# Kernel tuning notes

Measured on AMD Instinct MI355X. Metric: run time of the kernel, lower is better.

Reference implementation:

```python
import jax, jax.numpy as jnp
import numpy as np

B, S, H, V = 32, 128, 1024, 32000


def setup_inputs() -> dict:
    key = jax.random.key(0)
    ks = jax.random.split(key, 20)
    sc = 1.0 / np.sqrt(H)
    inp = {
        "inputs": jax.random.randint(ks[0], (B, S), 0, V),
        "annotations": jax.random.normal(ks[1], (B, S, H), dtype=jnp.float32),
        "hidden_init": jax.random.normal(ks[2], (B, H), dtype=jnp.float32),
        "E": jax.random.normal(ks[3], (V, H), dtype=jnp.float32) * sc,
        "Wxr": jax.random.normal(ks[4], (H, H), dtype=jnp.float32) * sc,
        "bxr": jnp.zeros((H,), jnp.float32),
        "Wxz": jax.random.normal(ks[5], (H, H), dtype=jnp.float32) * sc,
        "bxz": jnp.zeros((H,), jnp.float32),
        "Wxg": jax.random.normal(ks[6], (H, H), dtype=jnp.float32) * sc,
        "bxg": jnp.zeros((H,), jnp.float32),
        "Whr": jax.random.normal(ks[7], (H, H), dtype=jnp.float32) * sc,
        "bhr": jnp.zeros((H,), jnp.float32),
        "Whz": jax.random.normal(ks[8], (H, H), dtype=jnp.float32) * sc,
        "bhz": jnp.zeros((H,), jnp.float32),
        "Whg": jax.random.normal(ks[9], (H, H), dtype=jnp.float32) * sc,
        "bhg": jnp.zeros((H,), jnp.float32),
        "Wout": jax.random.normal(ks[10], (H, V), dtype=jnp.float32) * sc,
        "bout": jnp.zeros((V,), jnp.float32),
    }
    return inp


def reference(inputs, annotations, hidden_init, E, Wxr, bxr, Wxz, bxz, Wxg, bxg,
              Whr, bhr, Whz, bhz, Whg, bhg, Wout, bout):
    # annotations is unused (matches original non-attentional decoder).
    emb = E[inputs]  # [B, S, H]
    # Precompute all input-to-hidden projections as batched GEMMs (time-parallel).
    xr = jnp.einsum('bsh,hk->bsk', emb, Wxr) + bxr  # [B,S,H]
    xz = jnp.einsum('bsh,hk->bsk', emb, Wxz) + bxz
    xg = jnp.einsum('bsh,hk->bsk', emb, Wxg) + bxg
    # Scan over time for the sequential recurrence.
    xs = (jnp.swapaxes(xr, 0, 1), jnp.swapaxes(xz, 0, 1), jnp.swapaxes(xg, 0, 1))  # [S,B,H]

    def step(h, x):
        x_r, x_z, x_g = x
        r = jax.nn.sigmoid(x_r + h @ Whr + bhr)
        z = jax.nn.sigmoid(x_z + h @ Whz + bhz)
        g = jnp.tanh(x_g + r * (h @ Whg + bhg))
        h_new = (1.0 - z) * g + z * h
        return h_new, h_new

    _, hiddens = jax.lax.scan(step, hidden_init, xs)  # [S,B,H]
    hiddens = jnp.swapaxes(hiddens, 0, 1)  # [B,S,H]
    output = jnp.einsum('bsh,hv->bsv', hiddens, Wout) + bout  # [B,S,V]
    return output
```

## Files before the change

kernel.cpp:

```cpp
#include <hip/hip_runtime.h>
#include <hip/hip_bf16.h>

#define B_ 32
#define S_ 128
#define H_ 1024
#define V_ 32000

using short8 = __attribute__((ext_vector_type(8))) short;
using f32x4  = __attribute__((ext_vector_type(4))) float;
typedef unsigned short u16;

__device__ inline u16 f2bf(float f) {
  unsigned u = __float_as_uint(f);
  unsigned r = u + 0x7FFFu + ((u >> 16) & 1u);
  return (u16)(r >> 16);
}
__device__ inline float bf2f(u16 h) { return __uint_as_float(((unsigned)h) << 16); }

__device__ inline void gload_lds16(const void* g, void* l) {
  __builtin_amdgcn_global_load_lds((const __attribute__((address_space(1))) unsigned int*)g,
                                   (__attribute__((address_space(3))) unsigned int*)l, 16, 0, 0);
}
__device__ inline void gload_lds16_sc(const void* g, void* l) {
  __builtin_amdgcn_global_load_lds((const __attribute__((address_space(1))) unsigned int*)g,
                                   (__attribute__((address_space(3))) unsigned int*)l, 16, 0, 17);
}


__global__ void k_gather_embed(const int* __restrict__ idx, const float* __restrict__ E,
                               u16* __restrict__ embf) {
  int g = blockIdx.x * blockDim.x + threadIdx.x;
  int kt = g >> 14, rem = g & 16383, mt = rem >> 6, l = rem & 63;
  int row = mt * 16 + (l & 15);
  int k = kt * 32 + ((l >> 4) << 3);
  const float4* src = reinterpret_cast<const float4*>(E + (size_t)idx[row] * H_ + k);
  float4 a = src[0], b = src[1];
  u16 o[8] = {f2bf(a.x), f2bf(a.y), f2bf(a.z), f2bf(a.w),
              f2bf(b.x), f2bf(b.y), f2bf(b.z), f2bf(b.w)};
  *reinterpret_cast<uint4*>(embf + (size_t)g * 8) = *reinterpret_cast<const uint4*>(o);
}

__global__ void k_cvt_wx(const float* __restrict__ Wxr, const float* __restrict__ Wxz,
                         const float* __restrict__ Wxg, u16* __restrict__ wxf) {
  int g = blockIdx.x * blockDim.x + threadIdx.x;
  int kt = g / 12288, rem = g % 12288, nf = rem >> 6, l = rem & 63;
  int col = nf * 16 + (l & 15);
  int gate = col >> 10, j = col & 1023;
  int k0 = kt * 32 + ((l >> 4) << 3);
  const float* W = gate == 0 ? Wxr : (gate == 1 ? Wxz : Wxg);
  u16 o[8];
#pragma unroll
  for (int e = 0; e < 8; ++e) o[e] = f2bf(W[(size_t)(k0 + e) * H_ + j]);
  *reinterpret_cast<uint4*>(wxf + (size_t)g * 8) = *reinterpret_cast<const uint4*>(o);
}

__global__ void k_cvt_wout(const float* __restrict__ W, u16* __restrict__ wof) {
  int g = blockIdx.x * blockDim.x + threadIdx.x;
  int kt = g / 128000, rem = g - kt * 128000, nf = rem >> 6, l = rem & 63;
  int col = nf * 16 + (l & 15);
  int k0 = kt * 32 + ((l >> 4) << 3);
  u16 o[8];
#pragma unroll
  for (int e = 0; e < 8; ++e) o[e] = f2bf(W[(size_t)(k0 + e) * V_ + col]);
  *reinterpret_cast<uint4*>(wof + (size_t)g * 8) = *reinterpret_cast<const uint4*>(o);
}

__global__ void k_prep_wh(const float* __restrict__ Whr, const float* __restrict__ Whz,
                          const float* __restrict__ Whg, u16* __restrict__ whh,
                          u16* __restrict__ whl) {
  int g = blockIdx.x * blockDim.x + threadIdx.x;
  int jtile = g / 6144, rem = g % 6144;
  int gate = rem >> 11, kt = (rem >> 6) & 31, l = rem & 63;
  int col = jtile * 16 + (l & 15);
  int k0 = kt * 32 + ((l >> 4) << 3);
  const float* W = gate == 0 ? Whr : (gate == 1 ? Whz : Whg);
  u16 oh[8], ol[8];
#pragma unroll
  for (int e = 0; e < 8; ++e) {
    float v = W[(size_t)(k0 + e) * H_ + col];
    u16 hi = f2bf(v);
    oh[e] = hi;
    ol[e] = f2bf(v - bf2f(hi));
  }
  *reinterpret_cast<uint4*>(whh + (size_t)g * 8) = *reinterpret_cast<const uint4*>(oh);
  *reinterpret_cast<uint4*>(whl + (size_t)g * 8) = *reinterpret_cast<const uint4*>(ol);
}

__global__ void k_prep_h0(const float* __restrict__ h0, unsigned* __restrict__ hpack,
                          int* __restrict__ sync) {
  int i = blockIdx.x * blockDim.x + threadIdx.x;
  float v = h0[i];
  u16 hi = f2bf(v);
  hpack[i] = (unsigned)hi | ((unsigned)f2bf(v - bf2f(hi)) << 16);
  if (i < 8192) sync[i] = 0;
}

__global__ void k_bcat(const float* __restrict__ bxr, const float* __restrict__ bxz,
                       const float* __restrict__ bxg, float* __restrict__ bcat) {
  int j = blockIdx.x * blockDim.x + threadIdx.x;
  bcat[j] = j < 1024 ? bxr[j] : (j < 2048 ? bxz[j - 1024] : bxg[j - 2048]);
}

__launch_bounds__(256, 2)
__global__ void k_gemm_frag(const u16* __restrict__ Af, const u16* __restrict__ Bf,
                            const float* __restrict__ bias, float* __restrict__ C,
                            int MT, int NT, int KT, int N) {
  __shared__ __align__(16) u16 lA[2 * 512 * 8];
  __shared__ __align__(16) u16 lB[2 * 512 * 8];
  int tid = threadIdx.x, w = tid >> 6, lane = tid & 63;
  int mt0 = blockIdx.x * 8, nf0 = blockIdx.y * 8;
  int wm = (w >> 1) * 4, wn = (w & 1) * 4;
  f32x4 acc[4][4] = {};
  for (int kt = 0; kt < KT; kt += 2) {
    __syncthreads();
#pragma unroll
    for (int hh = 0; hh < 2; ++hh) {
      const u16* ga = Af + ((size_t)(kt + hh) * MT + mt0) * 512;
      const u16* gb = Bf + ((size_t)(kt + hh) * NT + nf0) * 512;
#pragma unroll
      for (int r = 0; r < 2; ++r) {
        int ub = (r * 4 + w) * 64;
        gload_lds16(ga + (size_t)(ub + lane) * 8, lA + (size_t)(hh * 512 + ub) * 8);
        gload_lds16(gb + (size_t)(ub + lane) * 8, lB + (size_t)(hh * 512 + ub) * 8);
      }
    }
    __syncthreads();
#pragma unroll
    for (int hh = 0; hh < 2; ++hh) {
      short8 af[4], bfr[4];
#pragma unroll
      for (int i = 0; i < 4; ++i) {
        af[i]  = *reinterpret_cast<const short8*>(lA + ((hh * 8 + wm + i) * 64 + lane) * 8);
        bfr[i] = *reinterpret_cast<const short8*>(lB + ((hh * 8 + wn + i) * 64 + lane) * 8);
      }
#pragma unroll
      for (int mi = 0; mi < 4; ++mi)
#pragma unroll
        for (int ni = 0; ni < 4; ++ni)
          acc[mi][ni] = __builtin_amdgcn_mfma_f32_16x16x32_bf16(af[mi], bfr[ni], acc[mi][ni], 0, 0, 0);
    }
  }
  int m0 = mt0 * 16, n0 = nf0 * 16;
#pragma unroll
  for (int ni = 0; ni < 4; ++ni) {
    int col = n0 + (wn + ni) * 16 + (lane & 15);
    float bv = bias[col];
#pragma unroll
    for (int mi = 0; mi < 4; ++mi) {
#pragma unroll
      for (int q = 0; q < 4; ++q) {
        int row = m0 + (wm + mi) * 16 + ((lane >> 4) << 2) + q;
        C[(size_t)row * N + col] = acc[mi][ni][q] + bv;
      }
    }
  }
}

__launch_bounds__(768, 3)
__global__ void k_gru_persist(const u16* __restrict__ whh, const u16* __restrict__ whl,
                              const float* __restrict__ xcat, const float* __restrict__ bhr,
                              const float* __restrict__ bhz, const float* __restrict__ bhg,
                              const float* __restrict__ hinit, unsigned* __restrict__ hpack,
                              u16* __restrict__ hiddf, int* __restrict__ sync) {
  __shared__ unsigned hstage[16][1028];
  __shared__ float red[3][4][16][16];
  const int tid = threadIdx.x;
  const int w = tid >> 6, l = tid & 63;
  const int mhalf = (int)blockIdx.x >> 6, jtile = (int)blockIdx.x & 63;
  const int gate = w >> 2, kg = w & 3;
  const int lr = l & 15, lc = (l >> 4) << 3;

  short8 bh[8], bl[8];
  {
    size_t wb = (size_t)(jtile * 3 + gate) * 32 * 512;
#pragma unroll
    for (int t = 0; t < 8; ++t) {
      size_t u = wb + ((size_t)(kg * 8 + t) * 64 + l) * 8;
      bh[t] = *reinterpret_cast<const short8*>(whh + u);
      bl[t] = *reinterpret_cast<const short8*>(whl + u);
    }
  }
#pragma unroll
  for (int t = 0; t < 8; ++t)
    asm volatile("" : "+v"(bh[t]), "+v"(bl[t]));

  const int erow = tid >> 4, ecol = tid & 15;
  const int eb = mhalf * 16 + erow, ej = jtile * 16 + ecol;
  const float* xp = xcat + (size_t)eb * S_ * 3072 + ej;
  float hprev = 0.f, br = 0.f, bz = 0.f, bg = 0.f, xr = 0.f, xz = 0.f, xg = 0.f;
  if (tid < 256) {
    hprev = hinit[(size_t)eb * H_ + ej];
    br = bhr[ej]; bz = bhz[ej]; bg = bhg[ej];
    xr = xp[0]; xz = xp[1024]; xg = xp[2048];
  }

  for (int s = 0; s < S_; ++s) {
    const int pi = s & 1, po = pi ^ 1;

    {
      const unsigned* hbase = hpack + (size_t)pi * (B_ * H_) + (size_t)(mhalf * 16) * H_;
      for (int c = w; c < 64; c += 12) {
        int r = c >> 2, q = c & 3;
        gload_lds16_sc(hbase + (size_t)r * H_ + q * 256 + l * 4, &hstage[r][q * 256]);
      }
    }
    __syncthreads();

    float nxr = 0.f, nxz = 0.f, nxg = 0.f;
    if (tid < 256 && s + 1 < S_) {
      const float* xq = xp + (size_t)(s + 1) * 3072;
      nxr = xq[0]; nxz = xq[1024]; nxg = xq[2048];
    }

    f32x4 acc = {};
#pragma unroll
    for (int t = 0; t < 8; ++t) {
      int c = (kg * 8 + t) * 32 + lc;
      uint4 A  = *reinterpret_cast<const uint4*>(&hstage[lr][c]);
      uint4 Bv = *reinterpret_cast<const uint4*>(&hstage[lr][c + 4]);
      union { unsigned u[4]; short8 s8; } ah, al;
      ah.u[0] = __builtin_amdgcn_perm(A.y, A.x, 0x05040100);
      al.u[0] = __builtin_amdgcn_perm(A.y, A.x, 0x07060302);
      ah.u[1] = __builtin_amdgcn_perm(A.w, A.z, 0x05040100);
      al.u[1] = __builtin_amdgcn_perm(A.w, A.z, 0x07060302);
      ah.u[2] = __builtin_amdgcn_perm(Bv.y, Bv.x, 0x05040100);
      al.u[2] = __builtin_amdgcn_perm(Bv.y, Bv.x, 0x07060302);
      ah.u[3] = __builtin_amdgcn_perm(Bv.w, Bv.z, 0x05040100);
      al.u[3] = __builtin_amdgcn_perm(Bv.w, Bv.z, 0x07060302);
      acc = __builtin_amdgcn_mfma_f32_16x16x32_bf16(ah.s8, bh[t], acc, 0, 0, 0);
      acc = __builtin_amdgcn_mfma_f32_16x16x32_bf16(ah.s8, bl[t], acc, 0, 0, 0);
      acc = __builtin_amdgcn_mfma_f32_16x16x32_bf16(al.s8, bh[t], acc, 0, 0, 0);
    }
#pragma unroll
    for (int q = 0; q < 4; ++q)
      red[gate][kg][(l >> 4) * 4 + q][lr] = acc[q];
    __syncthreads();

    if (tid < 256) {
      float ar = br + xr, az = bz + xz, ag = bg;
#pragma unroll
      for (int k2 = 0; k2 < 4; ++k2) {
        ar += red[0][k2][erow][ecol];
        az += red[1][k2][erow][ecol];
        ag += red[2][k2][erow][ecol];
      }
      float r = 1.f / (1.f + __expf(-ar));
      float z = 1.f / (1.f + __expf(-az));
      float ta = xg + r * ag;
      float gv = 1.f - 2.f / (__expf(2.f * ta) + 1.f);
      float hnew = (1.f - z) * gv + z * hprev;
      hprev = hnew;
      u16 hi = f2bf(hnew);
      u16 lo = f2bf(hnew - bf2f(hi));
      __hip_atomic_store(hpack + (size_t)po * (B_ * H_) + (size_t)eb * H_ + ej,
                         (unsigned)hi | ((unsigned)lo << 16),
                         __ATOMIC_RELAXED, __HIP_MEMORY_SCOPE_AGENT);
      int row = eb * S_ + s;
      int ktO = ej >> 5, mtO = row >> 4, laneO = (row & 15) + 16 * ((ej >> 3) & 3);
      hiddf[(((size_t)ktO * 256 + mtO) * 64 + laneO) * 8 + (ej & 7)] = hi;
    }
    xr = nxr; xz = nxz; xg = nxg;

    if (s + 1 < S_) {
      __syncthreads();
      if (tid == 0)
        __hip_atomic_store(sync + (int)blockIdx.x * 16, s + 1,
                           __ATOMIC_RELAXED, __HIP_MEMORY_SCOPE_AGENT);
      if (tid < 64) {
        const int* fp = sync + (mhalf * 64 + tid) * 16;
        while (__hip_atomic_load(fp, __ATOMIC_RELAXED, __HIP_MEMORY_SCOPE_AGENT) <= s)
          __builtin_amdgcn_s_sleep(1);
      }
      __syncthreads();
    }
  }
}

extern "C" void kernel_launch(void* const* d_in, const int* in_sizes, int n_in,
                              void* d_out, int out_size, void* d_ws, size_t ws_size,
                              hipStream_t stream) {
  const int*   inputs      = (const int*)d_in[0];
  const float* hidden_init = (const float*)d_in[2];
  const float* E    = (const float*)d_in[3];
  const float* Wxr  = (const float*)d_in[4];  const float* bxr = (const float*)d_in[5];
  const float* Wxz  = (const float*)d_in[6];  const float* bxz = (const float*)d_in[7];
  const float* Wxg  = (const float*)d_in[8];  const float* bxg = (const float*)d_in[9];
  const float* Whr  = (const float*)d_in[10]; const float* bhr = (const float*)d_in[11];
  const float* Whz  = (const float*)d_in[12]; const float* bhz = (const float*)d_in[13];
  const float* Whg  = (const float*)d_in[14]; const float* bhg = (const float*)d_in[15];
  const float* Wout = (const float*)d_in[16]; const float* bout = (const float*)d_in[17];
  float* out = (float*)d_out;

  char* ws = (char*)d_ws;
  u16* wxf       = (u16*)(ws);
  u16* wof       = (u16*)(ws + 6291456);
  u16* embf      = (u16*)(ws + 71827456);
  u16* hiddf     = embf;
  float* bcat    = (float*)(ws + 80216064);
  float* xcat    = (float*)(ws + 80228352);
  u16* whh       = (u16*)(ws + 130560000);
  u16* whl       = (u16*)(ws + 136851456);
  unsigned* hpack= (unsigned*)(ws + 143142912);
  int* syncb     = (int*)(ws + 143405056);

  k_gather_embed<<<2048, 256, 0, stream>>>(inputs, E, embf);
  k_cvt_wx<<<1536, 256, 0, stream>>>(Wxr, Wxz, Wxg, wxf);
  k_cvt_wout<<<16000, 256, 0, stream>>>(Wout, wof);
  k_prep_wh<<<1536, 256, 0, stream>>>(Whr, Whz, Whg, whh, whl);
  k_prep_h0<<<128, 256, 0, stream>>>(hidden_init, hpack, syncb);
  k_bcat<<<12, 256, 0, stream>>>(bxr, bxz, bxg, bcat);

  k_gemm_frag<<<dim3(32, 24), 256, 0, stream>>>(embf, wxf, bcat, xcat, 256, 192, 32, 3072);

  {
    const u16* whh_p = whh; const u16* whl_p = whl; const float* xcat_p = xcat;
    const float* bhr_p = bhr; const float* bhz_p = bhz; const float* bhg_p = bhg;
    const float* hinit_p = hidden_init; unsigned* hpack_p = hpack;
    u16* hiddf_p = hiddf; int* sync_p = syncb;
    void* kargs[] = {&whh_p, &whl_p, &xcat_p, &bhr_p, &bhz_p, &bhg_p,
                     &hinit_p, &hpack_p, &hiddf_p, &sync_p};
    hipLaunchCooperativeKernel((const void*)k_gru_persist, dim3(128), dim3(768),
                               kargs, 0, stream);
  }

  k_gemm_frag<<<dim3(32, 250), 256, 0, stream>>>(hiddf, wof, bout, out, 256, 2000, 32, 32000);
}
```

Measured before the change: 875.9 us.

## Replace GEMM with 256x256-tile double-buffered pipelined MFMA kernel

Replaces the 128x128-tile, 256-thread GEMM with a 256x256-tile, 512-thread kernel that double-buffers LDS, prefetching the next k-tile while computing the current one. It uses explicit vmcnt/lgkmcnt waits, barriers and setprio around the MFMA loop. Larger tiles raise arithmetic intensity per global load, and the pipeline is meant to hide load latency. In exchange there are fewer blocks (192 for the input projection) and more registers per thread, which could leave CUs idle or limit occupancy.

```diff
diff --git a/kernel.cpp b/kernel.cpp
--- a/kernel.cpp
+++ b/kernel.cpp
@@ -101,55 +101,69 @@
   bcat[j] = j < 1024 ? bxr[j] : (j < 2048 ? bxz[j - 1024] : bxg[j - 2048]);
 }
 
-__launch_bounds__(256, 2)
-__global__ void k_gemm_frag(const u16* __restrict__ Af, const u16* __restrict__ Bf,
-                            const float* __restrict__ bias, float* __restrict__ C,
-                            int MT, int NT, int KT, int N) {
-  __shared__ __align__(16) u16 lA[2 * 512 * 8];
-  __shared__ __align__(16) u16 lB[2 * 512 * 8];
-  int tid = threadIdx.x, w = tid >> 6, lane = tid & 63;
-  int mt0 = blockIdx.x * 8, nf0 = blockIdx.y * 8;
-  int wm = (w >> 1) * 4, wn = (w & 1) * 4;
-  f32x4 acc[4][4] = {};
-  for (int kt = 0; kt < KT; kt += 2) {
-    __syncthreads();
-#pragma unroll
-    for (int hh = 0; hh < 2; ++hh) {
-      const u16* ga = Af + ((size_t)(kt + hh) * MT + mt0) * 512;
-      const u16* gb = Bf + ((size_t)(kt + hh) * NT + nf0) * 512;
-#pragma unroll
-      for (int r = 0; r < 2; ++r) {
-        int ub = (r * 4 + w) * 64;
-        gload_lds16(ga + (size_t)(ub + lane) * 8, lA + (size_t)(hh * 512 + ub) * 8);
-        gload_lds16(gb + (size_t)(ub + lane) * 8, lB + (size_t)(hh * 512 + ub) * 8);
-      }
-    }
-    __syncthreads();
-#pragma unroll
-    for (int hh = 0; hh < 2; ++hh) {
-      short8 af[4], bfr[4];
-#pragma unroll
-      for (int i = 0; i < 4; ++i) {
-        af[i]  = *reinterpret_cast<const short8*>(lA + ((hh * 8 + wm + i) * 64 + lane) * 8);
-        bfr[i] = *reinterpret_cast<const short8*>(lB + ((hh * 8 + wn + i) * 64 + lane) * 8);
-      }
-#pragma unroll
-      for (int mi = 0; mi < 4; ++mi)
-#pragma unroll
-        for (int ni = 0; ni < 4; ++ni)
-          acc[mi][ni] = __builtin_amdgcn_mfma_f32_16x16x32_bf16(af[mi], bfr[ni], acc[mi][ni], 0, 0, 0);
-    }
-  }
-  int m0 = mt0 * 16, n0 = nf0 * 16;
+__launch_bounds__(512, 2)
+__global__ void k_gemm256(const u16* __restrict__ Af, const u16* __restrict__ Bf,
+                          const float* __restrict__ bias, float* __restrict__ C,
+                          int MT, int NT, int KT, int N) {
+  __shared__ __align__(16) u16 lA[2][16 * 512];
+  __shared__ __align__(16) u16 lB[2][16 * 512];
+  const int tid = threadIdx.x, w = tid >> 6, l = tid & 63;
+  const int mt0 = blockIdx.x * 16, nf0 = blockIdx.y * 16;
+  const int wm = (w & 1) * 8, wn = (w >> 1) * 4;
+  f32x4 acc[8][4] = {};
+
+#define STAGE256(kt_, buf_)                                                        \
+  {                                                                                \
+    const u16* ga = Af + ((size_t)(kt_) * MT + mt0) * 512;                         \
+    const u16* gb = Bf + ((size_t)(kt_) * NT + nf0) * 512;                         \
+    gload_lds16(ga + ((size_t)(w)*64 + l) * 8, &lA[buf_][((w)*64 + l) * 8]);       \
+    gload_lds16(ga + ((size_t)(8 + w) * 64 + l) * 8, &lA[buf_][((8 + w) * 64 + l) * 8]); \
+    gload_lds16(gb + ((size_t)(w)*64 + l) * 8, &lB[buf_][((w)*64 + l) * 8]);       \
+    gload_lds16(gb + ((size_t)(8 + w) * 64 + l) * 8, &lB[buf_][((8 + w) * 64 + l) * 8]); \
+  }
+
+  STAGE256(0, 0);
+  STAGE256(1, 1);
+
+  for (int kt = 0; kt < KT; ++kt) {
+    const int cur = kt & 1;
+    if (kt + 1 < KT) asm volatile("s_waitcnt vmcnt(4)" ::: "memory");
+    else             asm volatile("s_waitcnt vmcnt(0)" ::: "memory");
+    __builtin_amdgcn_s_barrier();
+
+    short8 af[8], bfr[4];
+#pragma unroll
+    for (int i = 0; i < 8; ++i)
+      af[i] = *reinterpret_cast<const short8*>(&lA[cur][((wm + i) * 64 + l) * 8]);
+#pragma unroll
+    for (int i = 0; i < 4; ++i)
+      bfr[i] = *reinterpret_cast<const short8*>(&lB[cur][((wn + i) * 64 + l) * 8]);
+    asm volatile("s_waitcnt lgkmcnt(0)" ::: "memory");
+    __builtin_amdgcn_sched_barrier(0);
+    __builtin_amdgcn_s_barrier();
+
+    if (kt + 2 < KT) STAGE256(kt + 2, cur);
+
+    __builtin_amdgcn_s_setprio(1);
+#pragma unroll
+    for (int mi = 0; mi < 8; ++mi)
+#pragma unroll
+      for (int ni = 0; ni < 4; ++ni)
+        acc[mi][ni] = __builtin_amdgcn_mfma_f32_16x16x32_bf16(af[mi], bfr[ni], acc[mi][ni], 0, 0, 0);
+    __builtin_amdgcn_s_setprio(0);
+  }
+#undef STAGE256
+
+  const int m0 = mt0 * 16, n0 = nf0 * 16;
 #pragma unroll
   for (int ni = 0; ni < 4; ++ni) {
-    int col = n0 + (wn + ni) * 16 + (lane & 15);
+    int col = n0 + (wn + ni) * 16 + (l & 15);
     float bv = bias[col];
 #pragma unroll
-    for (int mi = 0; mi < 4; ++mi) {
+    for (int mi = 0; mi < 8; ++mi) {
 #pragma unroll
       for (int q = 0; q < 4; ++q) {
-        int row = m0 + (wm + mi) * 16 + ((lane >> 4) << 2) + q;
+        int row = m0 + (wm + mi) * 16 + ((l >> 4) << 2) + q;
         C[(size_t)row * N + col] = acc[mi][ni][q] + bv;
       }
     }
@@ -310,7 +324,7 @@
   k_prep_h0<<<128, 256, 0, stream>>>(hidden_init, hpack, syncb);
   k_bcat<<<12, 256, 0, stream>>>(bxr, bxz, bxg, bcat);
 
-  k_gemm_frag<<<dim3(32, 24), 256, 0, stream>>>(embf, wxf, bcat, xcat, 256, 192, 32, 3072);
+  k_gemm256<<<dim3(16, 12), 512, 0, stream>>>(embf, wxf, bcat, xcat, 256, 192, 32, 3072);
 
   {
     const u16* whh_p = whh; const u16* whl_p = whl; const float* xcat_p = xcat;
@@ -323,5 +337,5 @@
                                kargs, 0, stream);
   }
 
-  k_gemm_frag<<<dim3(32, 250), 256, 0, stream>>>(hiddf, wof, bout, out, 256, 2000, 32, 32000);
-}
+  k_gemm256<<<dim3(16, 125), 512, 0, stream>>>(hiddf, wof, bout, out, 256, 2000, 32, 32000);
+}
```

After: 949.0 us. +8.3%, slower.
